# Performance work log

Hardware: AMD Instinct MI355X
Metric: run time of the kernel (lower is better)

## Reference

```python
import jax, jax.numpy as jnp
import numpy as np

B, R, L = 1, 128, 256
IN_DIM, DM, DIM = 128, 32, 128  # in_dim, dim_msa, dim


def setup_inputs() -> dict:
    key = jax.random.key(0)
    k = jax.random.split(key, 6)
    x = jax.random.normal(k[0], (B, L, L, DIM), dtype=jnp.float32)
    m = jax.random.normal(k[1], (B, R, L, IN_DIM), dtype=jnp.float32)
    # proj_down1: Linear(in_dim -> dim_msa)
    W1 = jax.random.normal(k[2], (DM, IN_DIM), dtype=jnp.float32) * (1.0 / np.sqrt(IN_DIM))
    b1 = jax.random.normal(k[3], (DM,), dtype=jnp.float32) * 0.02
    # proj_down2: Linear(dim_msa**2 -> dim)
    W2 = jax.random.normal(k[4], (DIM, DM * DM), dtype=jnp.float32) * (1.0 / DM)
    b2 = jax.random.normal(k[5], (DIM,), dtype=jnp.float32) * 0.02
    return {"x": x, "m": m, "W1": W1, "b1": b1, "W2": W2, "b2": b2}


def reference(x, m, W1, b1, W2, b2):
    # proj_down1: [b, r, i, in_dim] -> [b, r, i, dim_msa]
    mp = jnp.einsum('brie,de->brid', m, W1) + b1
    nrows = mp.shape[1]
    # Original math: outer = einsum('brid,brjc->bijcd', mp, mp)/nrows,
    # then rearrange 'b i j c d -> b i j (c d)' and Linear(dm^2 -> dim).
    # Flattened index (c d) => W2[k, c*DM + d]; fuse projection into the
    # contraction so the huge [b,i,j,c,d] tensor is never materialized.
    W2r = W2.reshape(DIM, DM, DM)  # (k, c, d)
    outer = jnp.einsum('brid,brjc,kcd->bijk', mp, mp, W2r) / nrows + b2
    return x + outer
```

## Files before the change

### kernel.cpp

```cpp
#include <hip/hip_runtime.h>
#include <stdint.h>


typedef __attribute__((ext_vector_type(8))) short bf16x8;
typedef __attribute__((ext_vector_type(4))) float f32x4;

#define MFMA16 __builtin_amdgcn_mfma_f32_16x16x32_bf16

__device__ __forceinline__ unsigned short f2bf(float f) {
    union { float f; unsigned int u; } x; x.f = f;
    unsigned int r = (x.u + 0x7fffu + ((x.u >> 16) & 1u)) >> 16;
    return (unsigned short)r;
}

__device__ __forceinline__ bf16x8 load8f_bf(const float* p) {
    float4 v0 = *(const float4*)p;
    float4 v1 = *(const float4*)(p + 4);
    union { bf16x8 v; unsigned short u[8]; } r;
    r.u[0] = f2bf(v0.x); r.u[1] = f2bf(v0.y); r.u[2] = f2bf(v0.z); r.u[3] = f2bf(v0.w);
    r.u[4] = f2bf(v1.x); r.u[5] = f2bf(v1.y); r.u[6] = f2bf(v1.z); r.u[7] = f2bf(v1.w);
    return r.v;
}

__global__ __launch_bounds__(256) void prep_kernel(
    const float* __restrict__ m, const float* __restrict__ W1,
    const float* __restrict__ pb1, const float* __restrict__ W2,
    unsigned short* __restrict__ mpF, unsigned short* __restrict__ W2f)
{
    const int bx = blockIdx.x;
    if (bx >= 512) {
        const int t    = (bx - 512) * 256 + threadIdx.x;
        const int nt   = t >> 11;
        const int kc   = (t >> 6) & 31;
        const int lane = t & 63;
        const int ln   = lane & 15, q = lane >> 4;
        const float* src = W2 + (size_t)(nt * 16 + ln) * 1024 + kc;
        union { bf16x8 v; unsigned short u[8]; } r;
        #pragma unroll
        for (int j = 0; j < 8; ++j)
            r.u[j] = f2bf(src[(q * 8 + j) * 32]);
        *(bf16x8*)(W2f + (size_t)t * 8) = r.v;
        return;
    }
    const int lane = threadIdx.x & 63;
    const int w    = threadIdx.x >> 6;
    const int ln   = lane & 15, q = lane >> 4;
    const int tile = bx * 4 + w;
    const int i    = tile >> 3;
    const int r0   = (tile & 7) * 16;

    const float* Ap  = m  + ((size_t)(r0 + ln) * 256 + i) * 128 + q * 8;
    const float* Bp0 = W1 + (size_t)ln * 128 + q * 8;
    const float* Bp1 = W1 + (size_t)(16 + ln) * 128 + q * 8;

    f32x4 acc0 = {0.f, 0.f, 0.f, 0.f};
    f32x4 acc1 = {0.f, 0.f, 0.f, 0.f};
    #pragma unroll
    for (int ke = 0; ke < 4; ++ke) {
        bf16x8 a  = load8f_bf(Ap  + ke * 32);
        bf16x8 b0 = load8f_bf(Bp0 + ke * 32);
        bf16x8 b1 = load8f_bf(Bp1 + ke * 32);
        acc0 = MFMA16(a, b0, acc0, 0, 0, 0);
        acc1 = MFMA16(a, b1, acc1, 0, 0, 0);
    }
    const float bb0 = pb1[ln];
    const float bb1 = pb1[16 + ln];
    const int kr = r0 >> 5;
    const int qr = ((r0 >> 4) & 1) * 2 + (q >> 1);
    const int j0 = (q & 1) * 4;
    const size_t off0 = (size_t)(i * 2 + 0) * 2048 + kr * 512 + (qr * 16 + ln) * 8 + j0;
    const size_t off1 = (size_t)(i * 2 + 1) * 2048 + kr * 512 + (qr * 16 + ln) * 8 + j0;
    ushort4 o0, o1;
    o0.x = f2bf(acc0[0] + bb0); o0.y = f2bf(acc0[1] + bb0);
    o0.z = f2bf(acc0[2] + bb0); o0.w = f2bf(acc0[3] + bb0);
    o1.x = f2bf(acc1[0] + bb1); o1.y = f2bf(acc1[1] + bb1);
    o1.z = f2bf(acc1[2] + bb1); o1.w = f2bf(acc1[3] + bb1);
    *(ushort4*)(mpF + off0) = o0;
    *(ushort4*)(mpF + off1) = o1;
}

__device__ __forceinline__ void stepB(const unsigned short* __restrict__ Ab,
                                      const unsigned short* __restrict__ Bb,
                                      f32x4 (&acc)[2][4])
{
    #pragma unroll
    for (int a = 0; a < 2; ++a)
        #pragma unroll
        for (int b = 0; b < 4; ++b)
            acc[a][b] = (f32x4){0.f, 0.f, 0.f, 0.f};
    #pragma unroll
    for (int ks = 0; ks < 4; ++ks) {
        bf16x8 av[2], bv[4];
        av[0] = *(const bf16x8*)(Ab + ks * 512);
        av[1] = *(const bf16x8*)(Ab + 2048 + ks * 512);
        #pragma unroll
        for (int bn = 0; bn < 4; ++bn)
            bv[bn] = *(const bf16x8*)(Bb + bn * 4096 + ks * 512);
        #pragma unroll
        for (int am = 0; am < 2; ++am)
            #pragma unroll
            for (int bn = 0; bn < 4; ++bn)
                acc[am][bn] = MFMA16(av[am], bv[bn], acc[am][bn], 0, 0, 0);
    }
}

__device__ __forceinline__ void gwrite(unsigned short* __restrict__ Gl,
                                       const f32x4 (&acc)[2][4],
                                       int ln, int q, int wm, int wn)
{
    #pragma unroll
    for (int am = 0; am < 2; ++am) {
        const int chunk = ln * 4 + am * 2 + (q >> 1);
        const int sig   = chunk >> 3;
        const int hbase = chunk * 256 + (q & 1) * 4;
        #pragma unroll
        for (int bn = 0; bn < 4; ++bn) {
            const int p  = (wn * 4 + bn) * 4 + wm;
            const int pp = p ^ sig;
            ushort4 g;
            g.x = f2bf(acc[am][bn][0]); g.y = f2bf(acc[am][bn][1]);
            g.z = f2bf(acc[am][bn][2]); g.w = f2bf(acc[am][bn][3]);
            *(ushort4*)(Gl + hbase + pp * 8) = g;
        }
    }
}

__device__ __forceinline__ void wpre(const unsigned short* __restrict__ wp, bf16x8 (&wv)[8])
{
    #pragma unroll
    for (int k8 = 0; k8 < 8; ++k8)
        wv[k8] = *(const bf16x8*)(wp + k8 * 512);
}

__device__ __forceinline__ void stepC(const unsigned short* __restrict__ Gl,
                                      const unsigned short* __restrict__ wp,
                                      bf16x8 (&wv)[8], int ln, int q,
                                      f32x4& c0, f32x4& c1)
{
    #pragma unroll
    for (int ks = 0; ks < 16; ++ks) {
        bf16x8 cur = wv[ks & 7];
        if (ks < 8) wv[ks & 7] = *(const bf16x8*)(wp + (ks + 8) * 512);
        const int chunk = ks * 4 + q;
        const int sig   = chunk >> 3;
        const unsigned short* gp = Gl + chunk * 256 + ((ln ^ sig) << 3);
        bf16x8 ag0 = *(const bf16x8*)gp;
        bf16x8 ag1 = *(const bf16x8*)(gp + 128);
        c0 = MFMA16(ag0, cur, c0, 0, 0, 0);
        c1 = MFMA16(ag1, cur, c1, 0, 0, 0);
    }
}

__global__ __launch_bounds__(512, 4) void fused_kernel(
    const float* __restrict__ x, const float* __restrict__ b2,
    const unsigned short* __restrict__ mpF, const unsigned short* __restrict__ W2f,
    float* __restrict__ out)
{
    __shared__ __align__(16) unsigned char smem[32768];
    unsigned short* Gl = (unsigned short*)smem;

    const int tid  = threadIdx.x;
    const int lane = tid & 63, w = tid >> 6;
    const int ln   = lane & 15, q = lane >> 4;
    const int wm   = w & 3, wn = w >> 2;

    const int i0 = blockIdx.x * 8;
    const int j0 = blockIdx.y * 8;

    const unsigned short* Ab0 = mpF + (size_t)((j0 + wm) * 2) * 2048 + lane * 8;
    const unsigned short* Ab1 = Ab0 + 16384;
    const unsigned short* Bb  = mpF + (size_t)((i0 + wn * 4) * 2) * 2048 + lane * 8;
    const unsigned short* wp0 = W2f + (size_t)(w * 32) * 512 + lane * 8;
    const unsigned short* wp1 = wp0 + 16 * 512;

    f32x4 cacc[4];
    #pragma unroll
    for (int t = 0; t < 4; ++t) cacc[t] = (f32x4){0.f, 0.f, 0.f, 0.f};
    f32x4 acc[2][4];
    bf16x8 wv[8];

    stepB(Ab0, Bb, acc);
    wpre(wp0, wv);
    gwrite(Gl, acc, ln, q, wm, wn);
    __syncthreads();
    stepC(Gl, wp0, wv, ln, q, cacc[0], cacc[1]);

    stepB(Ab1, Bb, acc);
    __syncthreads();
    wpre(wp0, wv);
    gwrite(Gl, acc, ln, q, wm, wn);
    __syncthreads();
    stepC(Gl, wp0, wv, ln, q, cacc[2], cacc[3]);

    stepB(Ab0, Bb + 2048, acc);
    __syncthreads();
    wpre(wp1, wv);
    gwrite(Gl, acc, ln, q, wm, wn);
    __syncthreads();
    stepC(Gl, wp1, wv, ln, q, cacc[0], cacc[1]);

    stepB(Ab1, Bb + 2048, acc);
    __syncthreads();
    wpre(wp1, wv);
    gwrite(Gl, acc, ln, q, wm, wn);
    __syncthreads();

    float4 xv[4];
    size_t gb[4];
    #pragma unroll
    for (int e = 0; e < 4; ++e) {
        const int fid = e * 512 + tid;
        const int po  = fid >> 5, kq = fid & 31;
        gb[e] = ((size_t)(i0 + (po >> 3)) * 256 + (j0 + (po & 7))) * 128 + kq * 4;
        xv[e] = *(const float4*)(x + gb[e]);
    }

    stepC(Gl, wp1, wv, ln, q, cacc[2], cacc[3]);
    __syncthreads();

    float* Ep = (float*)smem;
    const float invR = 1.0f / 128.0f;
    const int kk = w * 16 + ln;
    const int u  = kk >> 2, kl = kk & 3;
    #pragma unroll
    for (int jh = 0; jh < 2; ++jh)
        #pragma unroll
        for (int pt = 0; pt < 2; ++pt)
            #pragma unroll
            for (int rg = 0; rg < 4; ++rg) {
                const int po = (pt * 4 + q) * 8 + jh * 4 + rg;
                Ep[po * 128 + ((u ^ (po & 7)) << 2) + kl] = cacc[jh * 2 + pt][rg] * invR;
            }
    __syncthreads();

    #pragma unroll
    for (int e = 0; e < 4; ++e) {
        const int fid = e * 512 + tid;
        const int po  = fid >> 5, kq = fid & 31;
        const float4 v  = *(const float4*)(Ep + po * 128 + ((kq ^ (po & 7)) << 2));
        const float4 bv = *(const float4*)(b2 + kq * 4);
        float4 o;
        o.x = xv[e].x + v.x + bv.x; o.y = xv[e].y + v.y + bv.y;
        o.z = xv[e].z + v.z + bv.z; o.w = xv[e].w + v.w + bv.w;
        *(float4*)(out + gb[e]) = o;
    }
}

extern "C" void kernel_launch(void* const* d_in, const int* in_sizes, int n_in,
                              void* d_out, int out_size, void* d_ws, size_t ws_size,
                              hipStream_t stream) {
    const float* x  = (const float*)d_in[0];
    const float* m  = (const float*)d_in[1];
    const float* W1 = (const float*)d_in[2];
    const float* b1 = (const float*)d_in[3];
    const float* W2 = (const float*)d_in[4];
    const float* b2 = (const float*)d_in[5];
    float* out = (float*)d_out;

    unsigned short* mpF = (unsigned short*)d_ws;
    unsigned short* W2f = mpF + (size_t)512 * 2048;

    prep_kernel<<<dim3(576), dim3(256), 0, stream>>>(m, W1, b1, W2, mpF, W2f);
    fused_kernel<<<dim3(32, 32), dim3(512), 0, stream>>>(x, b2, mpF, W2f, out);
}
```

Baseline: 148.0 us.

## Double-buffer the LDS intermediate tile and raise wave priority around MFMA clusters

The fused kernel now alternates two 32KB LDS buffers for the per-phase intermediate tile. This lets it drop the barrier that guarded reuse of a single buffer before each write, and the barrier after the final contraction. It also wraps the MFMA groups in s_setprio raise/lower pairs and adds scheduling barriers between phases, so one wave's MFMAs can overlap other waves' loads. The cost is doubling the block's LDS footprint to 64KB, which may cut how many blocks fit on a CU below the requested launch bound.

```diff
diff --git a/kernel.cpp b/kernel.cpp
--- a/kernel.cpp
+++ b/kernel.cpp
@@ -96,11 +96,13 @@
         #pragma unroll
         for (int bn = 0; bn < 4; ++bn)
             bv[bn] = *(const bf16x8*)(Bb + bn * 4096 + ks * 512);
+        __builtin_amdgcn_s_setprio(1);
         #pragma unroll
         for (int am = 0; am < 2; ++am)
             #pragma unroll
             for (int bn = 0; bn < 4; ++bn)
                 acc[am][bn] = MFMA16(av[am], bv[bn], acc[am][bn], 0, 0, 0);
+        __builtin_amdgcn_s_setprio(0);
     }
 }
 
@@ -146,8 +148,10 @@
         const unsigned short* gp = Gl + chunk * 256 + ((ln ^ sig) << 3);
         bf16x8 ag0 = *(const bf16x8*)gp;
         bf16x8 ag1 = *(const bf16x8*)(gp + 128);
+        __builtin_amdgcn_s_setprio(1);
         c0 = MFMA16(ag0, cur, c0, 0, 0, 0);
         c1 = MFMA16(ag1, cur, c1, 0, 0, 0);
+        __builtin_amdgcn_s_setprio(0);
     }
 }
 
@@ -156,8 +160,9 @@
     const unsigned short* __restrict__ mpF, const unsigned short* __restrict__ W2f,
     float* __restrict__ out)
 {
-    __shared__ __align__(16) unsigned char smem[32768];
-    unsigned short* Gl = (unsigned short*)smem;
+    __shared__ __align__(16) unsigned char smem[65536];
+    unsigned short* Gl0 = (unsigned short*)smem;
+    unsigned short* Gl1 = (unsigned short*)(smem + 32768);
 
     const int tid  = threadIdx.x;
     const int lane = tid & 63, w = tid >> 6;
@@ -181,28 +186,28 @@
 
     stepB(Ab0, Bb, acc);
     wpre(wp0, wv);
-    gwrite(Gl, acc, ln, q, wm, wn);
-    __syncthreads();
-    stepC(Gl, wp0, wv, ln, q, cacc[0], cacc[1]);
+    gwrite(Gl0, acc, ln, q, wm, wn);
+    __syncthreads();
+    stepC(Gl0, wp0, wv, ln, q, cacc[0], cacc[1]);
+    __builtin_amdgcn_sched_barrier(0);
 
     stepB(Ab1, Bb, acc);
-    __syncthreads();
     wpre(wp0, wv);
-    gwrite(Gl, acc, ln, q, wm, wn);
-    __syncthreads();
-    stepC(Gl, wp0, wv, ln, q, cacc[2], cacc[3]);
+    gwrite(Gl1, acc, ln, q, wm, wn);
+    __syncthreads();
+    stepC(Gl1, wp0, wv, ln, q, cacc[2], cacc[3]);
+    __builtin_amdgcn_sched_barrier(0);
 
     stepB(Ab0, Bb + 2048, acc);
-    __syncthreads();
     wpre(wp1, wv);
-    gwrite(Gl, acc, ln, q, wm, wn);
-    __syncthreads();
-    stepC(Gl, wp1, wv, ln, q, cacc[0], cacc[1]);
+    gwrite(Gl0, acc, ln, q, wm, wn);
+    __syncthreads();
+    stepC(Gl0, wp1, wv, ln, q, cacc[0], cacc[1]);
+    __builtin_amdgcn_sched_barrier(0);
 
     stepB(Ab1, Bb + 2048, acc);
-    __syncthreads();
     wpre(wp1, wv);
-    gwrite(Gl, acc, ln, q, wm, wn);
+    gwrite(Gl1, acc, ln, q, wm, wn);
     __syncthreads();
 
     float4 xv[4];
@@ -215,8 +220,7 @@
         xv[e] = *(const float4*)(x + gb[e]);
     }
 
-    stepC(Gl, wp1, wv, ln, q, cacc[2], cacc[3]);
-    __syncthreads();
+    stepC(Gl1, wp1, wv, ln, q, cacc[2], cacc[3]);
 
     float* Ep = (float*)smem;
     const float invR = 1.0f / 128.0f;
```

Result: no change. 146.3 us (-1.2%).
